# Kernel tuning notes

Measured on AMD Instinct MI355X. Metric: run time of the kernel, lower is better.

## Reference

```python
import jax, jax.numpy as jnp
import numpy as np

D, HS, HE, E, K = 1024, 2048, 1024, 8, 2   # d_model, shared hidden (d_ff//2), expert hidden (d_ff//4), n_experts, top_k
B, T = 4, 1024
N_SHARED = 1


def setup_inputs() -> dict:
    key = jax.random.key(0)
    ks = jax.random.split(key, 9)
    g = lambda k, shape, s: jax.random.normal(k, shape, jnp.float32) * s
    return {
        "x": g(ks[0], (B, T, D), 1.0),
        "t_emb": g(ks[1], (B, D), 1.0),
        "router_W": g(ks[2], (2 * D, E), 0.01),      # torch Linear(2C->E, bias=False), std=0.01 init
        "router_bias": jnp.zeros((E,), jnp.float32),  # load-balance bias buffer
        "w1": g(ks[3], (D, HS), 0.02),                # shared expert SwiGLU
        "w3": g(ks[4], (D, HS), 0.02),
        "w2": g(ks[5], (HS, D), 0.02),
        "W1e": g(ks[6], (E, D, HE), 0.02),            # routed experts, Linear->GELU->Linear
        "W2e": g(ks[7], (E, HE, D), 0.02),
    }


def reference(x, t_emb, router_W, router_bias, w1, w3, w2, W1e, W2e):
    Bb, Tt, C = x.shape
    xf = x.reshape(-1, C)                                              # [N, C]
    tf = jnp.broadcast_to(t_emb[:, None, :], (Bb, Tt, C)).reshape(-1, C)
    N = xf.shape[0]

    shared = (jax.nn.silu(xf @ w1) * (xf @ w3)) @ w2                   # [N, C]

    # router affinity (sigmoid, fp32)
    s = jax.nn.sigmoid((jnp.concatenate([xf, tf], axis=-1) @ router_W).astype(jnp.float32))
    sel_scores = s + router_bias                                       # [N, E]
    _, topk_idx = jax.lax.top_k(sel_scores, K)                         # [N, K]

    # gates normalized over selected raw affinities
    s_sel = jnp.take_along_axis(s, topk_idx, axis=1)                   # [N, K]
    denom = s_sel.sum(axis=1, keepdims=True)
    gates = jnp.where(denom > 1e-9, s_sel / (denom + 1e-9), 1.0 / K).astype(x.dtype)

    # combine weights [N, E]: scatter gates to selected experts
    combine = jnp.zeros((N, E), x.dtype).at[jnp.arange(N)[:, None], topk_idx].add(gates)

    # dense expert evaluation (reference form of grouped GEMM + scatter-combine)
    h = jax.nn.gelu(jnp.einsum('nc,ech->enh', xf, W1e), approximate=False)  # [E, N, He]
    y = jnp.einsum('enh,ehc->enc', h, W2e)                                   # [E, N, C]
    routed = jnp.einsum('ne,enc->nc', combine, y)                            # [N, C]

    return ((shared + routed) / (N_SHARED + K)).reshape(Bb, Tt, C)
```

## Files before the change

### kernel.cpp

```cpp
#include <hip/hip_runtime.h>
#include <hip/hip_bf16.h>
#include <math.h>

#define D_MODEL 1024
#define HS 2048
#define HE 1024
#define NEXP 8
#define NTOK 4096
#define NSLOT 8192

typedef __attribute__((ext_vector_type(4))) float f32x4;
typedef __attribute__((ext_vector_type(8))) short bf16x8;

__device__ __forceinline__ short f2b(float f) {
  __hip_bfloat16 h = __float2bfloat16(f);
  return *reinterpret_cast<short*>(&h);
}
__device__ __forceinline__ float b2f(short s) {
  return __bfloat162float(*reinterpret_cast<__hip_bfloat16*>(&s));
}

__device__ __forceinline__ void gl_lds16(const short* g, short* l) {
  __builtin_amdgcn_global_load_lds(
      (const __attribute__((address_space(1))) void*)g,
      (__attribute__((address_space(3))) void*)l, 16, 0, 0);
}

__global__ __launch_bounds__(256) void cvt_x_kernel(const float* __restrict__ in,
                                                    short* __restrict__ out) {
  int i = blockIdx.x * 256 + threadIdx.x;
  const float4 v = ((const float4*)in)[i];
  short4 o;
  o.x = f2b(v.x); o.y = f2b(v.y); o.z = f2b(v.z); o.w = f2b(v.w);
  ((short4*)out)[i] = o;
}

template <int RMAP>
__global__ __launch_bounds__(256) void transpose_cvt(const float* __restrict__ in,
                                                     short* __restrict__ out,
                                                     int R, int C) {
  __shared__ float tile[64][69];
  const int t = threadIdx.x;
  const int c0 = blockIdx.x * 64;
  const int r0 = blockIdx.y * 64;
  const size_t bo = (size_t)blockIdx.z * R * C;
  const int lr = t >> 4;
  const int lc4 = (t & 15) * 4;
#pragma unroll
  for (int i = 0; i < 4; i++) {
    const float4 v = *(const float4*)&in[bo + (size_t)(r0 + lr + i * 16) * C + c0 + lc4];
    tile[lc4 + 0][lr + i * 16] = v.x;
    tile[lc4 + 1][lr + i * 16] = v.y;
    tile[lc4 + 2][lr + i * 16] = v.z;
    tile[lc4 + 3][lr + i * 16] = v.w;
  }
  __syncthreads();
#pragma unroll
  for (int i = 0; i < 4; i++) {
    const int oc = (t >> 4) + i * 16;
    const int or4 = (t & 15) * 4;
    short4 o;
    o.x = f2b(tile[oc][or4 + 0]);
    o.y = f2b(tile[oc][or4 + 1]);
    o.z = f2b(tile[oc][or4 + 2]);
    o.w = f2b(tile[oc][or4 + 3]);
    const int c = c0 + oc;
    size_t orow;
    if (RMAP == 0) orow = bo + (size_t)c * R;
    else orow = (size_t)((c >> 5) * 64 + (RMAP == 2 ? 32 : 0) + (c & 31)) * R;
    *(short4*)&out[orow + r0 + or4] = o;
  }
}

__global__ __launch_bounds__(256) void router_kernel(
    const float* __restrict__ x, const float* __restrict__ temb,
    const float* __restrict__ rw, const float* __restrict__ rbias,
    int* __restrict__ topk, float* __restrict__ gates) {
  const int t = (blockIdx.x * 256 + threadIdx.x) >> 6;
  const int lane = threadIdx.x & 63;
  const float* xr = x + (size_t)t * D_MODEL;
  const float* tr = temb + (size_t)(t >> 10) * D_MODEL;
  float acc[NEXP] = {};
#pragma unroll
  for (int i = 0; i < 4; i++) {
    const int j = i * 256 + lane * 4;
    const float4 xv = *(const float4*)&xr[j];
    const float4 tv = *(const float4*)&tr[j];
    const float* wx = rw + (size_t)j * NEXP;
    const float* wt = rw + (size_t)(D_MODEL + j) * NEXP;
    const float xa[4] = {xv.x, xv.y, xv.z, xv.w};
    const float ta[4] = {tv.x, tv.y, tv.z, tv.w};
#pragma unroll
    for (int u = 0; u < 4; u++)
#pragma unroll
      for (int e = 0; e < NEXP; e++)
        acc[e] += xa[u] * wx[u * NEXP + e] + ta[u] * wt[u * NEXP + e];
  }
#pragma unroll
  for (int off = 32; off; off >>= 1)
#pragma unroll
    for (int e = 0; e < NEXP; e++) acc[e] += __shfl_xor(acc[e], off);
  if (lane == 0) {
    float s[NEXP], sel[NEXP];
#pragma unroll
    for (int e = 0; e < NEXP; e++) {
      s[e] = 1.f / (1.f + expf(-acc[e]));
      sel[e] = s[e] + rbias[e];
    }
    int i0 = 0;
#pragma unroll
    for (int e = 1; e < NEXP; e++) if (sel[e] > sel[i0]) i0 = e;
    int i1 = (i0 == 0) ? 1 : 0;
#pragma unroll
    for (int e = 0; e < NEXP; e++) if (e != i0 && sel[e] > sel[i1]) i1 = e;
    float s0 = s[i0], s1 = s[i1], den = s0 + s1;
    float g0, g1;
    if (den > 1e-9f) { g0 = s0 / (den + 1e-9f); g1 = s1 / (den + 1e-9f); }
    else { g0 = 0.5f; g1 = 0.5f; }
    topk[t * 2] = i0; topk[t * 2 + 1] = i1;
    gates[t * 2] = g0; gates[t * 2 + 1] = g1;
  }
}

__global__ __launch_bounds__(1024) void group_kernel(const int* __restrict__ topk,
                                                     int* __restrict__ perm,
                                                     int* __restrict__ offs) {
  __shared__ int cnt[NEXP], cur[NEXP];
  const int t = threadIdx.x;
  if (t < NEXP) cnt[t] = 0;
  __syncthreads();
  int mye[8];
#pragma unroll
  for (int i = 0; i < 8; i++) {
    mye[i] = topk[i * 1024 + t];
    atomicAdd(&cnt[mye[i]], 1);
  }
  __syncthreads();
  if (t == 0) {
    int a = 0;
    for (int e = 0; e < NEXP; e++) { offs[e] = a; cur[e] = a; a += cnt[e]; }
    offs[NEXP] = a;
  }
  __syncthreads();
#pragma unroll
  for (int i = 0; i < 8; i++) {
    int pos = atomicAdd(&cur[mye[i]], 1);
    perm[pos] = i * 1024 + t;
  }
}

__global__ __launch_bounds__(512, 1) void gemm_g1_8ph(
    const short* __restrict__ A, const short* __restrict__ B, short* __restrict__ U) {
  extern __shared__ short lds[];
  const int td = threadIdx.x;
  const int bx = blockIdx.x;
  const int m0 = blockIdx.y * 256;
  const short* Bbase = B + (size_t)bx * 256 * 1024;

  const int srow = td >> 3;
  const int colsw8 = ((td & 7) ^ (srow & 7)) * 8;
  const short* ap[2][2];
  const short* bp[2][2];
#pragma unroll
  for (int h = 0; h < 2; h++)
#pragma unroll
    for (int i = 0; i < 2; i++) {
      const int trow = h * 128 + i * 64 + srow;
      ap[h][i] = A + (size_t)(m0 + trow) * 1024 + colsw8;
      bp[h][i] = Bbase + (size_t)trow * 1024 + colsw8;
    }

#define SB0(t_, b_)                                                        \
  do {                                                                     \
    gl_lds16(bp[0][0] + (t_) * 64, lds + (b_) * 32768 + 16384 + td * 8);   \
    gl_lds16(bp[0][1] + (t_) * 64, lds + (b_) * 32768 + 16384 + 4096 + td * 8); \
  } while (0)
#define SB1(t_, b_)                                                        \
  do {                                                                     \
    gl_lds16(bp[1][0] + (t_) * 64, lds + (b_) * 32768 + 16384 + 8192 + td * 8); \
    gl_lds16(bp[1][1] + (t_) * 64, lds + (b_) * 32768 + 16384 + 8192 + 4096 + td * 8); \
  } while (0)
#define SAI0(t_, b_)                                                       \
  do {                                                                     \
    gl_lds16(ap[0][0] + (t_) * 64, lds + (b_) * 32768 + td * 8);           \
    gl_lds16(ap[1][0] + (t_) * 64, lds + (b_) * 32768 + 8192 + td * 8);    \
  } while (0)
#define SAI1(t_, b_)                                                       \
  do {                                                                     \
    gl_lds16(ap[0][1] + (t_) * 64, lds + (b_) * 32768 + 4096 + td * 8);    \
    gl_lds16(ap[1][1] + (t_) * 64, lds + (b_) * 32768 + 8192 + 4096 + td * 8); \
  } while (0)

  const int l = td & 63;
  const int wid = td >> 6;
  const int mh = wid >> 2;
  const int wn4 = wid & 3;
  const int lr = l & 15;
  const int bhsel = wn4 >> 1;
  const int bnr = (wn4 & 1) * 64;
  const int swzk0 = ((0 + (l >> 4) * 16) ^ ((l & 7) << 4)) >> 1;
  const int swzk1 = ((64 + (l >> 4) * 16) ^ ((l & 7) << 4)) >> 1;

#define LDA(mf_, swz_) (*(const bf16x8*)&Ah[(unsigned)(((mf_)*16 + lr) * 64) + (swz_)])
#define LDB(nf_, swz_) (*(const bf16x8*)&Bh[(unsigned)((bnr + (nf_)*16 + lr) * 64) + (swz_)])
#define MMROW(mf_, a_)                                                                 \
  acc[mf_][0] = __builtin_amdgcn_mfma_f32_16x16x32_bf16(a_, b0, acc[mf_][0], 0, 0, 0); \
  acc[mf_][1] = __builtin_amdgcn_mfma_f32_16x16x32_bf16(a_, b1, acc[mf_][1], 0, 0, 0); \
  acc[mf_][2] = __builtin_amdgcn_mfma_f32_16x16x32_bf16(a_, b2, acc[mf_][2], 0, 0, 0); \
  acc[mf_][3] = __builtin_amdgcn_mfma_f32_16x16x32_bf16(a_, b3, acc[mf_][3], 0, 0, 0)

#define PH_TAIL                                   \
  __builtin_amdgcn_s_barrier();                   \
  asm volatile("s_waitcnt lgkmcnt(0)" ::: "memory"); \
  __builtin_amdgcn_sched_barrier(0);              \
  __builtin_amdgcn_s_setprio(1)
#define PH_END                                    \
  __builtin_amdgcn_s_setprio(0);                  \
  __builtin_amdgcn_s_barrier();                   \
  __builtin_amdgcn_sched_barrier(0)

  f32x4 acc[8][4] = {};

  SB0(0, 0); SB1(0, 0); SAI0(0, 0); SAI1(0, 0);
  asm volatile("s_waitcnt vmcnt(2)" ::: "memory");
  __builtin_amdgcn_s_barrier();

  for (int t = 0; t < 16; ++t) {
    const int p = t & 1, q = p ^ 1;
    const short* Ah = lds + p * 32768 + mh * 8192;
    const short* Bh = lds + p * 32768 + 16384 + bhsel * 8192;
    bf16x8 b0, b1, b2, b3, a0, a1, a2, a3;
    b0 = LDB(0, swzk0); b1 = LDB(1, swzk0); b2 = LDB(2, swzk0); b3 = LDB(3, swzk0);
    a0 = LDA(0, swzk0); a1 = LDA(1, swzk0); a2 = LDA(2, swzk0); a3 = LDA(3, swzk0);
    if (t < 15) {
      SB0(t + 1, q);
      asm volatile("s_waitcnt vmcnt(2)" ::: "memory");
    } else {
      asm volatile("s_waitcnt vmcnt(0)" ::: "memory");
    }
    PH_TAIL;
    MMROW(0, a0); MMROW(1, a1); MMROW(2, a2); MMROW(3, a3);
    PH_END;
    a0 = LDA(4, swzk0); a1 = LDA(5, swzk0); a2 = LDA(6, swzk0); a3 = LDA(7, swzk0);
    if (t < 15) SB1(t + 1, q);
    PH_TAIL;
    MMROW(4, a0); MMROW(5, a1); MMROW(6, a2); MMROW(7, a3);
    PH_END;
    b0 = LDB(0, swzk1); b1 = LDB(1, swzk1); b2 = LDB(2, swzk1); b3 = LDB(3, swzk1);
    a0 = LDA(0, swzk1); a1 = LDA(1, swzk1); a2 = LDA(2, swzk1); a3 = LDA(3, swzk1);
    if (t < 15) SAI0(t + 1, q);
    PH_TAIL;
    MMROW(0, a0); MMROW(1, a1); MMROW(2, a2); MMROW(3, a3);
    PH_END;
    a0 = LDA(4, swzk1); a1 = LDA(5, swzk1); a2 = LDA(6, swzk1); a3 = LDA(7, swzk1);
    if (t < 15) {
      SAI1(t + 1, q);
      asm volatile("s_waitcnt vmcnt(2)" ::: "memory");
    }
    PH_TAIL;
    MMROW(4, a0); MMROW(5, a1); MMROW(6, a2); MMROW(7, a3);
    PH_END;
  }

  const int rsub = (l >> 4) * 4;
#pragma unroll
  for (int mf = 0; mf < 8; mf++)
#pragma unroll
    for (int j = 0; j < 4; j++) {
      const int row = m0 + mh * 128 + mf * 16 + rsub + j;
      short* Up = U + (size_t)row * HS + bx * 128 + wn4 * 32 + lr;
#pragma unroll
      for (int nfp = 0; nfp < 2; nfp++) {
        const float a = acc[mf][nfp][j];
        const float b = acc[mf][nfp + 2][j];
        Up[nfp * 16] = f2b(a / (1.f + expf(-a)) * b);
      }
    }
#undef SB0
#undef SB1
#undef SAI0
#undef SAI1
#undef LDA
#undef LDB
#undef MMROW
#undef PH_TAIL
#undef PH_END
}

template <int MODE>
__global__ __launch_bounds__(256, 2) void gemm_grouped(
    const short* __restrict__ A, const short* __restrict__ B, short* __restrict__ C,
    const int* __restrict__ perm, const int* __restrict__ offs,
    const float* __restrict__ gates) {
  __shared__ __align__(16) short As[4096];
  __shared__ __align__(16) short Bs[4096];
  const int t = threadIdx.x;
  const int tile_n = blockIdx.x * 128;
  const int m0 = blockIdx.y * 128;
  const int e = blockIdx.z;
  const int rbeg = offs[e], rend = offs[e + 1];
  if (m0 >= rend - rbeg) return;
  const int K = (MODE == 1) ? D_MODEL : HE;
  const short* Bp = B + (size_t)e * (size_t)HE * D_MODEL;

  const int r = t >> 2;
  const int c8 = (t & 3) * 8;
  size_t arow0, arow1;
  {
    int gi0 = min(rbeg + m0 + r, rend - 1);
    int gi1 = min(rbeg + m0 + 64 + r, rend - 1);
    if (MODE == 1) {
      arow0 = (size_t)(perm[gi0] >> 1) * K;
      arow1 = (size_t)(perm[gi1] >> 1) * K;
    } else {
      arow0 = (size_t)gi0 * K;
      arow1 = (size_t)gi1 * K;
    }
  }
  const short* Ap0 = A + arow0 + c8;
  const short* Ap1 = A + arow1 + c8;
  const short* Bp0 = Bp + (size_t)(tile_n + r) * K + c8;
  const short* Bp1 = Bp + (size_t)(tile_n + 64 + r) * K + c8;

  const int lane = t & 63, wv = t >> 6;
  const int wm = (wv >> 1) * 64, wn = (wv & 1) * 64;
  const int lr = lane & 15, lk = (lane >> 4) * 8;

  f32x4 acc[4][4] = {};
  for (int k0 = 0; k0 < K; k0 += 32) {
    gl_lds16(Ap0 + k0, &As[t * 8]);
    gl_lds16(Ap1 + k0, &As[2048 + t * 8]);
    gl_lds16(Bp0 + k0, &Bs[t * 8]);
    gl_lds16(Bp1 + k0, &Bs[2048 + t * 8]);
    __syncthreads();
    bf16x8 af[4], bfr[4];
#pragma unroll
    for (int m = 0; m < 4; m++) af[m] = *(const bf16x8*)&As[(wm + m * 16 + lr) * 32 + lk];
#pragma unroll
    for (int n = 0; n < 4; n++) bfr[n] = *(const bf16x8*)&Bs[(wn + n * 16 + lr) * 32 + lk];
#pragma unroll
    for (int m = 0; m < 4; m++)
#pragma unroll
      for (int n = 0; n < 4; n++)
        acc[m][n] = __builtin_amdgcn_mfma_f32_16x16x32_bf16(af[m], bfr[n], acc[m][n], 0, 0, 0);
    __syncthreads();
  }

  const int rq = (lane >> 4) * 4;
#pragma unroll
  for (int m = 0; m < 4; m++) {
#pragma unroll
    for (int j = 0; j < 4; j++) {
      const int gi = rbeg + m0 + wm + m * 16 + rq + j;
      if (gi < rend) {
        if (MODE == 1) {
          short* Cp = C + (size_t)gi * HE + tile_n + wn + lr;
#pragma unroll
          for (int n = 0; n < 4; n++) {
            float v = acc[m][n][j];
            Cp[n * 16] = f2b(0.5f * v * (1.0f + erff(v * 0.70710678118654752f)));
          }
        } else {
          const int slot = perm[gi];
          const float g = gates[slot];
          short* Cp = C + (size_t)slot * D_MODEL + tile_n + wn + lr;
#pragma unroll
          for (int n = 0; n < 4; n++) Cp[n * 16] = f2b(g * acc[m][n][j]);
        }
      }
    }
  }
}

__global__ __launch_bounds__(256, 2) void gemm_g2(
    const short* __restrict__ A, const short* __restrict__ B,
    const short* __restrict__ yb, float* __restrict__ out) {
  __shared__ __align__(16) short As[4096];
  __shared__ __align__(16) short Bs[4096];
  const int t = threadIdx.x;
  const int tile_n = blockIdx.x * 128;
  const int m0 = blockIdx.y * 128;
  const int r = t >> 2;
  const int c8 = (t & 3) * 8;
  const short* Ap0 = A + (size_t)(m0 + r) * HS + c8;
  const short* Ap1 = A + (size_t)(m0 + 64 + r) * HS + c8;
  const short* Bp0 = B + (size_t)(tile_n + r) * HS + c8;
  const short* Bp1 = B + (size_t)(tile_n + 64 + r) * HS + c8;

  const int lane = t & 63, wv = t >> 6;
  const int wm = (wv >> 1) * 64, wn = (wv & 1) * 64;
  const int lr = lane & 15, lk = (lane >> 4) * 8;

  f32x4 acc[4][4] = {};
  for (int k0 = 0; k0 < HS; k0 += 32) {
    gl_lds16(Ap0 + k0, &As[t * 8]);
    gl_lds16(Ap1 + k0, &As[2048 + t * 8]);
    gl_lds16(Bp0 + k0, &Bs[t * 8]);
    gl_lds16(Bp1 + k0, &Bs[2048 + t * 8]);
    __syncthreads();
    bf16x8 af[4], bfr[4];
#pragma unroll
    for (int m = 0; m < 4; m++) af[m] = *(const bf16x8*)&As[(wm + m * 16 + lr) * 32 + lk];
#pragma unroll
    for (int n = 0; n < 4; n++) bfr[n] = *(const bf16x8*)&Bs[(wn + n * 16 + lr) * 32 + lk];
#pragma unroll
    for (int m = 0; m < 4; m++)
#pragma unroll
      for (int n = 0; n < 4; n++)
        acc[m][n] = __builtin_amdgcn_mfma_f32_16x16x32_bf16(af[m], bfr[n], acc[m][n], 0, 0, 0);
    __syncthreads();
  }

  const int rq = (lane >> 4) * 4;
  const float inv3 = 1.0f / 3.0f;
#pragma unroll
  for (int m = 0; m < 4; m++) {
#pragma unroll
    for (int j = 0; j < 4; j++) {
      const int tok = m0 + wm + m * 16 + rq + j;
      const int colb = tile_n + wn + lr;
      const short* y0p = yb + (size_t)(tok * 2) * D_MODEL + colb;
      const short* y1p = yb + (size_t)(tok * 2 + 1) * D_MODEL + colb;
      float* Op = out + (size_t)tok * D_MODEL + colb;
#pragma unroll
      for (int n = 0; n < 4; n++) {
        Op[n * 16] = (acc[m][n][j] + b2f(y0p[n * 16]) + b2f(y1p[n * 16])) * inv3;
      }
    }
  }
}

extern "C" void kernel_launch(void* const* d_in, const int* in_sizes, int n_in,
                              void* d_out, int out_size, void* d_ws, size_t ws_size,
                              hipStream_t stream) {
  const float* x = (const float*)d_in[0];
  const float* temb = (const float*)d_in[1];
  const float* rw = (const float*)d_in[2];
  const float* rbias = (const float*)d_in[3];
  const float* w1 = (const float*)d_in[4];
  const float* w3 = (const float*)d_in[5];
  const float* w2 = (const float*)d_in[6];
  const float* W1e = (const float*)d_in[7];
  const float* W2e = (const float*)d_in[8];
  float* out = (float*)d_out;

  const size_t MB = 1ull << 20;
  char* w = (char*)d_ws;
  short* xb    = (short*)(w + 0 * MB);
  short* w13I  = (short*)(w + 8 * MB);
  short* w2T   = (short*)(w + 16 * MB);
  short* W1eT  = (short*)(w + 20 * MB);
  short* W2eT  = (short*)(w + 36 * MB);
  short* ubuf  = (short*)(w + 52 * MB);
  short* hexpb = (short*)(w + 68 * MB);
  short* yb    = (short*)(w + 84 * MB);
  float* gates = (float*)(w + 100 * MB);
  int* topk    = (int*)(w + 100 * MB + 32 * 1024);
  int* perm    = (int*)(w + 100 * MB + 64 * 1024);
  int* offs    = (int*)(w + 100 * MB + 96 * 1024);

  hipFuncSetAttribute((const void*)&gemm_g1_8ph,
                      hipFuncAttributeMaxDynamicSharedMemorySize, 131072);

  cvt_x_kernel<<<NTOK * D_MODEL / 4 / 256, 256, 0, stream>>>(x, xb);
  transpose_cvt<1><<<dim3(HS / 64, D_MODEL / 64, 1), 256, 0, stream>>>(w1, w13I, D_MODEL, HS);
  transpose_cvt<2><<<dim3(HS / 64, D_MODEL / 64, 1), 256, 0, stream>>>(w3, w13I, D_MODEL, HS);
  transpose_cvt<0><<<dim3(D_MODEL / 64, HS / 64, 1), 256, 0, stream>>>(w2, w2T, HS, D_MODEL);
  transpose_cvt<0><<<dim3(HE / 64, D_MODEL / 64, NEXP), 256, 0, stream>>>(W1e, W1eT, D_MODEL, HE);
  transpose_cvt<0><<<dim3(D_MODEL / 64, HE / 64, NEXP), 256, 0, stream>>>(W2e, W2eT, HE, D_MODEL);

  router_kernel<<<NTOK / 4, 256, 0, stream>>>(x, temb, rw, rbias, topk, gates);
  group_kernel<<<1, 1024, 0, stream>>>(topk, perm, offs);

  gemm_g1_8ph<<<dim3(HS / 128, NTOK / 256, 1), 512, 131072, stream>>>(xb, w13I, ubuf);

  gemm_grouped<1><<<dim3(HE / 128, NSLOT / 128, NEXP), 256, 0, stream>>>(
      xb, W1eT, hexpb, perm, offs, gates);
  gemm_grouped<2><<<dim3(D_MODEL / 128, NSLOT / 128, NEXP), 256, 0, stream>>>(
      hexpb, W2eT, yb, perm, offs, gates);

  gemm_g2<<<dim3(D_MODEL / 128, NTOK / 128, 1), 256, 0, stream>>>(ubuf, w2T, yb, out);
}
```

Before: 252.1 us.

## Reuse 8-phase 256x256 GEMM for routed experts and fuse prep kernels

Replaces the simple 128x128 grouped expert GEMMs with the pipelined 8-phase 256x256 kernel (templated over modes for shared, expert-up with GELU and expert-down with gate scaling), using perm-indexed row gathers. It also merges the x conversion, all weight transposes and the router into a single prep launch to cut launch overhead. The larger tiles waste more work on ragged per-expert row counts, and the merged prep kernel runs blocks with very different workloads.

```diff
diff --git a/kernel.cpp b/kernel.cpp
--- a/kernel.cpp
+++ b/kernel.cpp
@@ -26,24 +26,13 @@
       (__attribute__((address_space(3))) void*)l, 16, 0, 0);
 }
 
-__global__ __launch_bounds__(256) void cvt_x_kernel(const float* __restrict__ in,
-                                                    short* __restrict__ out) {
-  int i = blockIdx.x * 256 + threadIdx.x;
-  const float4 v = ((const float4*)in)[i];
-  short4 o;
-  o.x = f2b(v.x); o.y = f2b(v.y); o.z = f2b(v.z); o.w = f2b(v.w);
-  ((short4*)out)[i] = o;
-}
-
-template <int RMAP>
-__global__ __launch_bounds__(256) void transpose_cvt(const float* __restrict__ in,
-                                                     short* __restrict__ out,
-                                                     int R, int C) {
-  __shared__ float tile[64][69];
-  const int t = threadIdx.x;
-  const int c0 = blockIdx.x * 64;
-  const int r0 = blockIdx.y * 64;
-  const size_t bo = (size_t)blockIdx.z * R * C;
+
+__device__ void transpose_tile(const float* __restrict__ in, short* __restrict__ out,
+                               int R, int C, int bx, int by, int bz, int rmap,
+                               float (*tile)[69], int t) {
+  const int c0 = bx * 64;
+  const int r0 = by * 64;
+  const size_t bo = (size_t)bz * R * C;
   const int lr = t >> 4;
   const int lc4 = (t & 15) * 4;
 #pragma unroll
@@ -66,18 +55,18 @@
     o.w = f2b(tile[oc][or4 + 3]);
     const int c = c0 + oc;
     size_t orow;
-    if (RMAP == 0) orow = bo + (size_t)c * R;
-    else orow = (size_t)((c >> 5) * 64 + (RMAP == 2 ? 32 : 0) + (c & 31)) * R;
+    if (rmap == 0) orow = bo + (size_t)c * R;
+    else orow = (size_t)((c >> 5) * 64 + (rmap == 2 ? 32 : 0) + (c & 31)) * R;
     *(short4*)&out[orow + r0 + or4] = o;
   }
 }
 
-__global__ __launch_bounds__(256) void router_kernel(
-    const float* __restrict__ x, const float* __restrict__ temb,
-    const float* __restrict__ rw, const float* __restrict__ rbias,
-    int* __restrict__ topk, float* __restrict__ gates) {
-  const int t = (blockIdx.x * 256 + threadIdx.x) >> 6;
-  const int lane = threadIdx.x & 63;
+__device__ void router_block(const float* __restrict__ x, const float* __restrict__ temb,
+                             const float* __restrict__ rw, const float* __restrict__ rbias,
+                             int* __restrict__ topk, float* __restrict__ gates,
+                             int bb, int tid) {
+  const int t = (bb * 256 + tid) >> 6;
+  const int lane = tid & 63;
   const float* xr = x + (size_t)t * D_MODEL;
   const float* tr = temb + (size_t)(t >> 10) * D_MODEL;
   float acc[NEXP] = {};
@@ -122,6 +111,47 @@
   }
 }
 
+__global__ __launch_bounds__(256) void prep_kernel(
+    const float* __restrict__ x, const float* __restrict__ temb,
+    const float* __restrict__ rw, const float* __restrict__ rbias,
+    const float* __restrict__ w1, const float* __restrict__ w3,
+    const float* __restrict__ w2, const float* __restrict__ W1e,
+    const float* __restrict__ W2e,
+    short* __restrict__ xb, short* __restrict__ w13I, short* __restrict__ w2T,
+    short* __restrict__ W1eT, short* __restrict__ W2eT,
+    int* __restrict__ topk, float* __restrict__ gates) {
+  __shared__ float tile[64][69];
+  const int b = blockIdx.x;
+  const int t = threadIdx.x;
+  if (b < 2048) {
+    const size_t base = ((size_t)b * 256 + t) * 8;
+    const float4 v0 = *(const float4*)&x[base];
+    const float4 v1 = *(const float4*)&x[base + 4];
+    short4 o0, o1;
+    o0.x = f2b(v0.x); o0.y = f2b(v0.y); o0.z = f2b(v0.z); o0.w = f2b(v0.w);
+    o1.x = f2b(v1.x); o1.y = f2b(v1.y); o1.z = f2b(v1.z); o1.w = f2b(v1.w);
+    *(short4*)&xb[base] = o0;
+    *(short4*)&xb[base + 4] = o1;
+  } else if (b < 2560) {
+    const int bb = b - 2048;
+    transpose_tile(w1, w13I, D_MODEL, HS, bb & 31, bb >> 5, 0, 1, tile, t);
+  } else if (b < 3072) {
+    const int bb = b - 2560;
+    transpose_tile(w3, w13I, D_MODEL, HS, bb & 31, bb >> 5, 0, 2, tile, t);
+  } else if (b < 3584) {
+    const int bb = b - 3072;
+    transpose_tile(w2, w2T, HS, D_MODEL, bb & 15, bb >> 4, 0, 0, tile, t);
+  } else if (b < 5632) {
+    const int bb = b - 3584;
+    transpose_tile(W1e, W1eT, D_MODEL, HE, bb & 15, (bb >> 4) & 15, bb >> 8, 0, tile, t);
+  } else if (b < 7680) {
+    const int bb = b - 5632;
+    transpose_tile(W2e, W2eT, HE, D_MODEL, bb & 15, (bb >> 4) & 15, bb >> 8, 0, tile, t);
+  } else {
+    router_block(x, temb, rw, rbias, topk, gates, b - 7680, t);
+  }
+}
+
 __global__ __launch_bounds__(1024) void group_kernel(const int* __restrict__ topk,
                                                      int* __restrict__ perm,
                                                      int* __restrict__ offs) {
@@ -149,13 +179,25 @@
   }
 }
 
-__global__ __launch_bounds__(512, 1) void gemm_g1_8ph(
-    const short* __restrict__ A, const short* __restrict__ B, short* __restrict__ U) {
+template <int MODE>
+__global__ __launch_bounds__(512, 1) void moe_gemm_8ph(
+    const short* __restrict__ A, const short* __restrict__ B, short* __restrict__ U,
+    const int* __restrict__ perm, const int* __restrict__ offs,
+    const float* __restrict__ gates) {
   extern __shared__ short lds[];
   const int td = threadIdx.x;
   const int bx = blockIdx.x;
   const int m0 = blockIdx.y * 256;
-  const short* Bbase = B + (size_t)bx * 256 * 1024;
+  int rbeg = 0, rend = 0;
+  const short* Bbase;
+  if (MODE == 0) {
+    Bbase = B + (size_t)bx * 256 * 1024;
+  } else {
+    const int e = blockIdx.z;
+    rbeg = offs[e]; rend = offs[e + 1];
+    if (m0 >= rend - rbeg) return;
+    Bbase = B + ((size_t)e * 1024 + bx * 256) * 1024;
+  }
 
   const int srow = td >> 3;
   const int colsw8 = ((td & 7) ^ (srow & 7)) * 8;
@@ -166,7 +208,11 @@
 #pragma unroll
     for (int i = 0; i < 2; i++) {
       const int trow = h * 128 + i * 64 + srow;
-      ap[h][i] = A + (size_t)(m0 + trow) * 1024 + colsw8;
+      int grow;
+      if (MODE == 0) grow = m0 + trow;
+      else if (MODE == 1) grow = perm[min(rbeg + m0 + trow, rend - 1)] >> 1;
+      else grow = min(rbeg + m0 + trow, rend - 1);
+      ap[h][i] = A + (size_t)grow * 1024 + colsw8;
       bp[h][i] = Bbase + (size_t)trow * 1024 + colsw8;
     }
 
@@ -263,19 +309,50 @@
   }
 
   const int rsub = (l >> 4) * 4;
-#pragma unroll
-  for (int mf = 0; mf < 8; mf++)
-#pragma unroll
-    for (int j = 0; j < 4; j++) {
-      const int row = m0 + mh * 128 + mf * 16 + rsub + j;
-      short* Up = U + (size_t)row * HS + bx * 128 + wn4 * 32 + lr;
-#pragma unroll
-      for (int nfp = 0; nfp < 2; nfp++) {
-        const float a = acc[mf][nfp][j];
-        const float b = acc[mf][nfp + 2][j];
-        Up[nfp * 16] = f2b(a / (1.f + expf(-a)) * b);
+  if (MODE == 0) {
+#pragma unroll
+    for (int mf = 0; mf < 8; mf++)
+#pragma unroll
+      for (int j = 0; j < 4; j++) {
+        const int row = m0 + mh * 128 + mf * 16 + rsub + j;
+        short* Up = U + (size_t)row * HS + bx * 128 + wn4 * 32 + lr;
+#pragma unroll
+        for (int nfp = 0; nfp < 2; nfp++) {
+          const float a = acc[mf][nfp][j];
+          const float b = acc[mf][nfp + 2][j];
+          Up[nfp * 16] = f2b(a / (1.f + expf(-a)) * b);
+        }
       }
-    }
+  } else if (MODE == 1) {
+#pragma unroll
+    for (int mf = 0; mf < 8; mf++)
+#pragma unroll
+      for (int j = 0; j < 4; j++) {
+        const int gi = rbeg + m0 + mh * 128 + mf * 16 + rsub + j;
+        if (gi < rend) {
+          short* Cp = U + (size_t)gi * HE + bx * 256 + wn4 * 64 + lr;
+#pragma unroll
+          for (int nf = 0; nf < 4; nf++) {
+            const float v = acc[mf][nf][j];
+            Cp[nf * 16] = f2b(0.5f * v * (1.0f + erff(v * 0.70710678118654752f)));
+          }
+        }
+      }
+  } else {
+#pragma unroll
+    for (int mf = 0; mf < 8; mf++)
+#pragma unroll
+      for (int j = 0; j < 4; j++) {
+        const int gi = rbeg + m0 + mh * 128 + mf * 16 + rsub + j;
+        if (gi < rend) {
+          const int slot = perm[gi];
+          const float g = gates[slot];
+          short* Cp = U + (size_t)slot * D_MODEL + bx * 256 + wn4 * 64 + lr;
+#pragma unroll
+          for (int nf = 0; nf < 4; nf++) Cp[nf * 16] = f2b(g * acc[mf][nf][j]);
+        }
+      }
+  }
 #undef SB0
 #undef SB1
 #undef SAI0
@@ -285,91 +362,6 @@
 #undef MMROW
 #undef PH_TAIL
 #undef PH_END
-}
-
-template <int MODE>
-__global__ __launch_bounds__(256, 2) void gemm_grouped(
-    const short* __restrict__ A, const short* __restrict__ B, short* __restrict__ C,
-    const int* __restrict__ perm, const int* __restrict__ offs,
-    const float* __restrict__ gates) {
-  __shared__ __align__(16) short As[4096];
-  __shared__ __align__(16) short Bs[4096];
-  const int t = threadIdx.x;
-  const int tile_n = blockIdx.x * 128;
-  const int m0 = blockIdx.y * 128;
-  const int e = blockIdx.z;
-  const int rbeg = offs[e], rend = offs[e + 1];
-  if (m0 >= rend - rbeg) return;
-  const int K = (MODE == 1) ? D_MODEL : HE;
-  const short* Bp = B + (size_t)e * (size_t)HE * D_MODEL;
-
-  const int r = t >> 2;
-  const int c8 = (t & 3) * 8;
-  size_t arow0, arow1;
-  {
-    int gi0 = min(rbeg + m0 + r, rend - 1);
-    int gi1 = min(rbeg + m0 + 64 + r, rend - 1);
-    if (MODE == 1) {
-      arow0 = (size_t)(perm[gi0] >> 1) * K;
-      arow1 = (size_t)(perm[gi1] >> 1) * K;
-    } else {
-      arow0 = (size_t)gi0 * K;
-      arow1 = (size_t)gi1 * K;
-    }
-  }
-  const short* Ap0 = A + arow0 + c8;
-  const short* Ap1 = A + arow1 + c8;
-  const short* Bp0 = Bp + (size_t)(tile_n + r) * K + c8;
-  const short* Bp1 = Bp + (size_t)(tile_n + 64 + r) * K + c8;
-
-  const int lane = t & 63, wv = t >> 6;
-  const int wm = (wv >> 1) * 64, wn = (wv & 1) * 64;
-  const int lr = lane & 15, lk = (lane >> 4) * 8;
-
-  f32x4 acc[4][4] = {};
-  for (int k0 = 0; k0 < K; k0 += 32) {
-    gl_lds16(Ap0 + k0, &As[t * 8]);
-    gl_lds16(Ap1 + k0, &As[2048 + t * 8]);
-    gl_lds16(Bp0 + k0, &Bs[t * 8]);
-    gl_lds16(Bp1 + k0, &Bs[2048 + t * 8]);
-    __syncthreads();
-    bf16x8 af[4], bfr[4];
-#pragma unroll
-    for (int m = 0; m < 4; m++) af[m] = *(const bf16x8*)&As[(wm + m * 16 + lr) * 32 + lk];
-#pragma unroll
-    for (int n = 0; n < 4; n++) bfr[n] = *(const bf16x8*)&Bs[(wn + n * 16 + lr) * 32 + lk];
-#pragma unroll
-    for (int m = 0; m < 4; m++)
-#pragma unroll
-      for (int n = 0; n < 4; n++)
-        acc[m][n] = __builtin_amdgcn_mfma_f32_16x16x32_bf16(af[m], bfr[n], acc[m][n], 0, 0, 0);
-    __syncthreads();
-  }
-
-  const int rq = (lane >> 4) * 4;
-#pragma unroll
-  for (int m = 0; m < 4; m++) {
-#pragma unroll
-    for (int j = 0; j < 4; j++) {
-      const int gi = rbeg + m0 + wm + m * 16 + rq + j;
-      if (gi < rend) {
-        if (MODE == 1) {
-          short* Cp = C + (size_t)gi * HE + tile_n + wn + lr;
-#pragma unroll
-          for (int n = 0; n < 4; n++) {
-            float v = acc[m][n][j];
-            Cp[n * 16] = f2b(0.5f * v * (1.0f + erff(v * 0.70710678118654752f)));
-          }
-        } else {
-          const int slot = perm[gi];
-          const float g = gates[slot];
-          short* Cp = C + (size_t)slot * D_MODEL + tile_n + wn + lr;
-#pragma unroll
-          for (int n = 0; n < 4; n++) Cp[n * 16] = f2b(g * acc[m][n][j]);
-        }
-      }
-    }
-  }
 }
 
 __global__ __launch_bounds__(256, 2) void gemm_g2(
@@ -459,24 +451,23 @@
   int* perm    = (int*)(w + 100 * MB + 64 * 1024);
   int* offs    = (int*)(w + 100 * MB + 96 * 1024);
 
-  hipFuncSetAttribute((const void*)&gemm_g1_8ph,
+  hipFuncSetAttribute((const void*)&moe_gemm_8ph<0>,
                       hipFuncAttributeMaxDynamicSharedMemorySize, 131072);
-
-  cvt_x_kernel<<<NTOK * D_MODEL / 4 / 256, 256, 0, stream>>>(x, xb);
-  transpose_cvt<1><<<dim3(HS / 64, D_MODEL / 64, 1), 256, 0, stream>>>(w1, w13I, D_MODEL, HS);
-  transpose_cvt<2><<<dim3(HS / 64, D_MODEL / 64, 1), 256, 0, stream>>>(w3, w13I, D_MODEL, HS);
-  transpose_cvt<0><<<dim3(D_MODEL / 64, HS / 64, 1), 256, 0, stream>>>(w2, w2T, HS, D_MODEL);
-  transpose_cvt<0><<<dim3(HE / 64, D_MODEL / 64, NEXP), 256, 0, stream>>>(W1e, W1eT, D_MODEL, HE);
-  transpose_cvt<0><<<dim3(D_MODEL / 64, HE / 64, NEXP), 256, 0, stream>>>(W2e, W2eT, HE, D_MODEL);
-
-  router_kernel<<<NTOK / 4, 256, 0, stream>>>(x, temb, rw, rbias, topk, gates);
+  hipFuncSetAttribute((const void*)&moe_gemm_8ph<1>,
+                      hipFuncAttributeMaxDynamicSharedMemorySize, 131072);
+  hipFuncSetAttribute((const void*)&moe_gemm_8ph<2>,
+                      hipFuncAttributeMaxDynamicSharedMemorySize, 131072);
+
+  prep_kernel<<<8704, 256, 0, stream>>>(x, temb, rw, rbias, w1, w3, w2, W1e, W2e,
+                                        xb, w13I, w2T, W1eT, W2eT, topk, gates);
   group_kernel<<<1, 1024, 0, stream>>>(topk, perm, offs);
 
-  gemm_g1_8ph<<<dim3(HS / 128, NTOK / 256, 1), 512, 131072, stream>>>(xb, w13I, ubuf);
-
-  gemm_grouped<1><<<dim3(HE / 128, NSLOT / 128, NEXP), 256, 0, stream>>>(
+  moe_gemm_8ph<0><<<dim3(HS / 128, NTOK / 256, 1), 512, 131072, stream>>>(
+      xb, w13I, ubuf, nullptr, nullptr, nullptr);
+
+  moe_gemm_8ph<1><<<dim3(HE / 256, 32, NEXP), 512, 131072, stream>>>(
       xb, W1eT, hexpb, perm, offs, gates);
-  gemm_grouped<2><<<dim3(D_MODEL / 128, NSLOT / 128, NEXP), 256, 0, stream>>>(
+  moe_gemm_8ph<2><<<dim3(D_MODEL / 256, 32, NEXP), 512, 131072, stream>>>(
       hexpb, W2eT, yb, perm, offs, gates);
 
   gemm_g2<<<dim3(D_MODEL / 128, NTOK / 128, 1), 256, 0, stream>>>(ubuf, w2T, yb, out);
```

New measurement: 304.6 us. 1.21x slower.

## Rewrite grouped expert GEMMs as triple-buffered 8-phase pipelined 128x256 tiles

Applied to the files above, without the earlier changes.

Replaces the simple single-buffered grouped expert GEMM, which synchronises twice per 32-wide K step, with a 512-thread kernel. The new kernel uses 128x256 tiles, a 64-wide K step, three LDS buffers with XOR-swizzled layout and async global-to-LDS prefetch two stages ahead. Each K step is split into phases with barriers and s_setprio so that MFMA work overlaps the loads. It mirrors the existing shared-expert 8-phase kernel. The costs are 144KB of LDS per block (one block per CU) and a hardcoded K of 1024, which is valid here for both modes.

```diff
diff --git a/kernel.cpp b/kernel.cpp
--- a/kernel.cpp
+++ b/kernel.cpp
@@ -288,88 +288,139 @@
 }
 
 template <int MODE>
-__global__ __launch_bounds__(256, 2) void gemm_grouped(
-    const short* __restrict__ A, const short* __restrict__ B, short* __restrict__ C,
+__global__ __launch_bounds__(512, 1) void moe_grp_8ph(
+    const short* __restrict__ A, const short* __restrict__ B, short* __restrict__ Cout,
     const int* __restrict__ perm, const int* __restrict__ offs,
     const float* __restrict__ gates) {
-  __shared__ __align__(16) short As[4096];
-  __shared__ __align__(16) short Bs[4096];
-  const int t = threadIdx.x;
-  const int tile_n = blockIdx.x * 128;
+  extern __shared__ short lds[];
+  const int td = threadIdx.x;
+  const int bx = blockIdx.x;
   const int m0 = blockIdx.y * 128;
   const int e = blockIdx.z;
   const int rbeg = offs[e], rend = offs[e + 1];
   if (m0 >= rend - rbeg) return;
-  const int K = (MODE == 1) ? D_MODEL : HE;
-  const short* Bp = B + (size_t)e * (size_t)HE * D_MODEL;
-
-  const int r = t >> 2;
-  const int c8 = (t & 3) * 8;
-  size_t arow0, arow1;
-  {
-    int gi0 = min(rbeg + m0 + r, rend - 1);
-    int gi1 = min(rbeg + m0 + 64 + r, rend - 1);
-    if (MODE == 1) {
-      arow0 = (size_t)(perm[gi0] >> 1) * K;
-      arow1 = (size_t)(perm[gi1] >> 1) * K;
+  const short* Bbase = B + ((size_t)e * 1024 + bx * 256) * 1024;
+
+  const int srow = td >> 3;
+  const int colsw8 = ((td & 7) ^ (srow & 7)) * 8;
+  const short* apx[2];
+  const short* bpx[4];
+#pragma unroll
+  for (int i = 0; i < 2; i++) {
+    const int trow = i * 64 + srow;
+    int grow;
+    if (MODE == 1) grow = perm[min(rbeg + m0 + trow, rend - 1)] >> 1;
+    else grow = min(rbeg + m0 + trow, rend - 1);
+    apx[i] = A + (size_t)grow * 1024 + colsw8;
+  }
+#pragma unroll
+  for (int u = 0; u < 4; u++)
+    bpx[u] = Bbase + (size_t)(u * 64 + srow) * 1024 + colsw8;
+
+#define SA(i_, t_, b_) gl_lds16(apx[i_] + (t_) * 64, lds + (b_) * 24576 + (i_) * 4096 + td * 8)
+#define SB(u_, t_, b_) gl_lds16(bpx[u_] + (t_) * 64, lds + (b_) * 24576 + 8192 + (u_) * 4096 + td * 8)
+
+  const int l = td & 63;
+  const int wid = td >> 6;
+  const int mh = wid >> 2;
+  const int wn4 = wid & 3;
+  const int lr = l & 15;
+  const int swzk0 = ((0 + (l >> 4) * 16) ^ ((l & 7) << 4)) >> 1;
+  const int swzk1 = ((64 + (l >> 4) * 16) ^ ((l & 7) << 4)) >> 1;
+
+#define LDA(mf_, swz_) (*(const bf16x8*)&Ah[(unsigned)(((mf_)*16 + lr) * 64) + (swz_)])
+#define LDB(nf_, swz_) (*(const bf16x8*)&Bh[(unsigned)(((nf_)*16 + lr) * 64) + (swz_)])
+#define MMROW(mf_, a_)                                                                 \
+  acc[mf_][0] = __builtin_amdgcn_mfma_f32_16x16x32_bf16(a_, b0, acc[mf_][0], 0, 0, 0); \
+  acc[mf_][1] = __builtin_amdgcn_mfma_f32_16x16x32_bf16(a_, b1, acc[mf_][1], 0, 0, 0); \
+  acc[mf_][2] = __builtin_amdgcn_mfma_f32_16x16x32_bf16(a_, b2, acc[mf_][2], 0, 0, 0); \
+  acc[mf_][3] = __builtin_amdgcn_mfma_f32_16x16x32_bf16(a_, b3, acc[mf_][3], 0, 0, 0)
+
+#define PH_TAIL                                   \
+  __builtin_amdgcn_s_barrier();                   \
+  asm volatile("s_waitcnt lgkmcnt(0)" ::: "memory"); \
+  __builtin_amdgcn_sched_barrier(0);              \
+  __builtin_amdgcn_s_setprio(1)
+#define PH_END                                    \
+  __builtin_amdgcn_s_setprio(0);                  \
+  __builtin_amdgcn_s_barrier();                   \
+  __builtin_amdgcn_sched_barrier(0)
+
+  f32x4 acc[4][4] = {};
+
+  SA(0, 0, 0); SA(1, 0, 0); SB(0, 0, 0); SB(1, 0, 0); SB(2, 0, 0); SB(3, 0, 0);
+  SA(0, 1, 1); SA(1, 1, 1); SB(0, 1, 1); SB(1, 1, 1); SB(2, 1, 1); SB(3, 1, 1);
+  asm volatile("s_waitcnt vmcnt(6)" ::: "memory");
+  __builtin_amdgcn_s_barrier();
+
+  int pb = 0;
+  int sb = 2;
+  for (int t = 0; t < 16; ++t) {
+    const short* Ah = lds + pb * 24576 + mh * 4096;
+    const short* Bh = lds + pb * 24576 + 8192 + wn4 * 4096;
+    bf16x8 b0, b1, b2, b3, a0, a1;
+    b0 = LDB(0, swzk0); b1 = LDB(1, swzk0); b2 = LDB(2, swzk0); b3 = LDB(3, swzk0);
+    a0 = LDA(0, swzk0); a1 = LDA(1, swzk0);
+    if (t <= 13) { SB(0, t + 2, sb); SB(1, t + 2, sb); }
+    PH_TAIL;
+    MMROW(0, a0); MMROW(1, a1);
+    PH_END;
+    a0 = LDA(2, swzk0); a1 = LDA(3, swzk0);
+    if (t <= 13) { SB(2, t + 2, sb); SB(3, t + 2, sb); }
+    PH_TAIL;
+    MMROW(2, a0); MMROW(3, a1);
+    PH_END;
+    b0 = LDB(0, swzk1); b1 = LDB(1, swzk1); b2 = LDB(2, swzk1); b3 = LDB(3, swzk1);
+    a0 = LDA(0, swzk1); a1 = LDA(1, swzk1);
+    if (t <= 13) { SA(0, t + 2, sb); SA(1, t + 2, sb); }
+    PH_TAIL;
+    MMROW(0, a0); MMROW(1, a1);
+    PH_END;
+    a0 = LDA(2, swzk1); a1 = LDA(3, swzk1);
+    PH_TAIL;
+    MMROW(2, a0); MMROW(3, a1);
+    __builtin_amdgcn_s_setprio(0);
+    if (t < 14) {
+      asm volatile("s_waitcnt vmcnt(6)" ::: "memory");
     } else {
-      arow0 = (size_t)gi0 * K;
-      arow1 = (size_t)gi1 * K;
-    }
-  }
-  const short* Ap0 = A + arow0 + c8;
-  const short* Ap1 = A + arow1 + c8;
-  const short* Bp0 = Bp + (size_t)(tile_n + r) * K + c8;
-  const short* Bp1 = Bp + (size_t)(tile_n + 64 + r) * K + c8;
-
-  const int lane = t & 63, wv = t >> 6;
-  const int wm = (wv >> 1) * 64, wn = (wv & 1) * 64;
-  const int lr = lane & 15, lk = (lane >> 4) * 8;
-
-  f32x4 acc[4][4] = {};
-  for (int k0 = 0; k0 < K; k0 += 32) {
-    gl_lds16(Ap0 + k0, &As[t * 8]);
-    gl_lds16(Ap1 + k0, &As[2048 + t * 8]);
-    gl_lds16(Bp0 + k0, &Bs[t * 8]);
-    gl_lds16(Bp1 + k0, &Bs[2048 + t * 8]);
-    __syncthreads();
-    bf16x8 af[4], bfr[4];
-#pragma unroll
-    for (int m = 0; m < 4; m++) af[m] = *(const bf16x8*)&As[(wm + m * 16 + lr) * 32 + lk];
-#pragma unroll
-    for (int n = 0; n < 4; n++) bfr[n] = *(const bf16x8*)&Bs[(wn + n * 16 + lr) * 32 + lk];
-#pragma unroll
-    for (int m = 0; m < 4; m++)
-#pragma unroll
-      for (int n = 0; n < 4; n++)
-        acc[m][n] = __builtin_amdgcn_mfma_f32_16x16x32_bf16(af[m], bfr[n], acc[m][n], 0, 0, 0);
-    __syncthreads();
-  }
-
-  const int rq = (lane >> 4) * 4;
-#pragma unroll
-  for (int m = 0; m < 4; m++) {
+      asm volatile("s_waitcnt vmcnt(0)" ::: "memory");
+    }
+    __builtin_amdgcn_s_barrier();
+    __builtin_amdgcn_sched_barrier(0);
+    pb = (pb == 2) ? 0 : pb + 1;
+    sb = (sb == 2) ? 0 : sb + 1;
+  }
+
+  const int rsub = (l >> 4) * 4;
+#pragma unroll
+  for (int mf = 0; mf < 4; mf++)
 #pragma unroll
     for (int j = 0; j < 4; j++) {
-      const int gi = rbeg + m0 + wm + m * 16 + rq + j;
+      const int gi = rbeg + m0 + mh * 64 + mf * 16 + rsub + j;
       if (gi < rend) {
         if (MODE == 1) {
-          short* Cp = C + (size_t)gi * HE + tile_n + wn + lr;
-#pragma unroll
-          for (int n = 0; n < 4; n++) {
-            float v = acc[m][n][j];
-            Cp[n * 16] = f2b(0.5f * v * (1.0f + erff(v * 0.70710678118654752f)));
+          short* Cp = Cout + (size_t)gi * HE + bx * 256 + wn4 * 64 + lr;
+#pragma unroll
+          for (int nf = 0; nf < 4; nf++) {
+            const float v = acc[mf][nf][j];
+            Cp[nf * 16] = f2b(0.5f * v * (1.0f + erff(v * 0.70710678118654752f)));
           }
         } else {
           const int slot = perm[gi];
           const float g = gates[slot];
-          short* Cp = C + (size_t)slot * D_MODEL + tile_n + wn + lr;
-#pragma unroll
-          for (int n = 0; n < 4; n++) Cp[n * 16] = f2b(g * acc[m][n][j]);
+          short* Cp = Cout + (size_t)slot * D_MODEL + bx * 256 + wn4 * 64 + lr;
+#pragma unroll
+          for (int nf = 0; nf < 4; nf++) Cp[nf * 16] = f2b(g * acc[mf][nf][j]);
         }
       }
     }
-  }
+#undef SA
+#undef SB
+#undef LDA
+#undef LDB
+#undef MMROW
+#undef PH_TAIL
+#undef PH_END
 }
 
 __global__ __launch_bounds__(256, 2) void gemm_g2(
@@ -461,6 +512,10 @@
 
   hipFuncSetAttribute((const void*)&gemm_g1_8ph,
                       hipFuncAttributeMaxDynamicSharedMemorySize, 131072);
+  hipFuncSetAttribute((const void*)&moe_grp_8ph<1>,
+                      hipFuncAttributeMaxDynamicSharedMemorySize, 147456);
+  hipFuncSetAttribute((const void*)&moe_grp_8ph<2>,
+                      hipFuncAttributeMaxDynamicSharedMemorySize, 147456);
 
   cvt_x_kernel<<<NTOK * D_MODEL / 4 / 256, 256, 0, stream>>>(x, xb);
   transpose_cvt<1><<<dim3(HS / 64, D_MODEL / 64, 1), 256, 0, stream>>>(w1, w13I, D_MODEL, HS);
@@ -468,15 +523,14 @@
   transpose_cvt<0><<<dim3(D_MODEL / 64, HS / 64, 1), 256, 0, stream>>>(w2, w2T, HS, D_MODEL);
   transpose_cvt<0><<<dim3(HE / 64, D_MODEL / 64, NEXP), 256, 0, stream>>>(W1e, W1eT, D_MODEL, HE);
   transpose_cvt<0><<<dim3(D_MODEL / 64, HE / 64, NEXP), 256, 0, stream>>>(W2e, W2eT, HE, D_MODEL);
-
   router_kernel<<<NTOK / 4, 256, 0, stream>>>(x, temb, rw, rbias, topk, gates);
   group_kernel<<<1, 1024, 0, stream>>>(topk, perm, offs);
 
   gemm_g1_8ph<<<dim3(HS / 128, NTOK / 256, 1), 512, 131072, stream>>>(xb, w13I, ubuf);
 
-  gemm_grouped<1><<<dim3(HE / 128, NSLOT / 128, NEXP), 256, 0, stream>>>(
+  moe_grp_8ph<1><<<dim3(HE / 256, NSLOT / 128, NEXP), 512, 147456, stream>>>(
       xb, W1eT, hexpb, perm, offs, gates);
-  gemm_grouped<2><<<dim3(D_MODEL / 128, NSLOT / 128, NEXP), 256, 0, stream>>>(
+  moe_grp_8ph<2><<<dim3(D_MODEL / 256, NSLOT / 128, NEXP), 512, 147456, stream>>>(
       hexpb, W2eT, yb, perm, offs, gates);
 
   gemm_g2<<<dim3(D_MODEL / 128, NTOK / 128, 1), 256, 0, stream>>>(ubuf, w2T, yb, out);
```

New measurement: 253.7 us. No clear change (+0.7%).
